# Optimization experiments

Measured on AMD Instinct MI355X. Metric: run time of the kernel, lower is better.

The kernel has to match this reference:

```python
import jax, jax.numpy as jnp
import numpy as np

B, S, H, NH, L = 2, 2048, 2048, 16, 512
HD = H // NH  # head_dim = 128


def setup_inputs() -> dict:
    key = jax.random.key(0)
    k1, k2, k3, k4, k5 = jax.random.split(key, 5)
    scale = 0.02  # mimic xavier-scale init
    return {
        "q": jax.random.normal(k1, (B, S, H), dtype=jnp.float32),
        "latent_kv": jax.random.normal(k2, (B, S, L), dtype=jnp.float32),
        "Wq": jax.random.normal(k3, (H, H), dtype=jnp.float32) * scale,
        "Wkv_expand": jax.random.normal(k4, (2 * H, L), dtype=jnp.float32) * scale,
        "Wout": jax.random.normal(k5, (H, H), dtype=jnp.float32) * scale,
    }


def reference(q, latent_kv, Wq, Wkv_expand, Wout):
    b, sq, _ = q.shape
    sk = latent_kv.shape[1]
    # projections (torch Linear: x @ W.T)
    qp = q @ Wq.T                              # [B,Sq,H]
    kv = latent_kv @ Wkv_expand.T              # [B,Sk,2H]
    k, v = jnp.split(kv, 2, axis=-1)           # each [B,Sk,H]
    # split heads -> [B,NH,S,HD]
    qh = qp.reshape(b, sq, NH, HD).transpose(0, 2, 1, 3)
    kh = k.reshape(b, sk, NH, HD).transpose(0, 2, 1, 3)
    vh = v.reshape(b, sk, NH, HD).transpose(0, 2, 1, 3)
    inv_sqrt_d = 1.0 / jnp.sqrt(jnp.float32(HD))
    scores = jnp.einsum("bhqd,bhkd->bhqk", qh, kh) * inv_sqrt_d
    # causal mask (seq_q == seq_k)
    causal = jnp.tril(jnp.ones((sq, sk), dtype=bool))
    scores = jnp.where(causal, scores, jnp.finfo(scores.dtype).min)
    attn = jax.nn.softmax(scores, axis=-1)
    out = jnp.einsum("bhqk,bhkd->bhqd", attn, vh)  # [B,NH,Sq,HD]
    out = out.transpose(0, 2, 1, 3).reshape(b, sq, H)
    return out @ Wout.T
```

## Files before the change

### kernel.cpp

```cpp
#include <hip/hip_runtime.h>

#define SLEN 2048
#define NHEADS 16
#define HDIM 128

typedef __attribute__((ext_vector_type(8))) short bf16x8;
typedef __attribute__((ext_vector_type(4))) float f32x4;
typedef __attribute__((ext_vector_type(16))) float f32x16;

__device__ __forceinline__ unsigned short f2bf(float f) {
  union { float f; unsigned u; } v; v.f = f;
  unsigned r = v.u + 0x7FFFu + ((v.u >> 16) & 1u);
  return (unsigned short)(r >> 16);
}

__device__ __forceinline__ float bf2f(unsigned short h) {
  union { unsigned u; float f; } v; v.u = (unsigned)h << 16;
  return v.f;
}

__device__ __forceinline__ unsigned pkbf(float a, float b) {
  unsigned r;
  asm("v_cvt_pk_bf16_f32 %0, %1, %2" : "=v"(r) : "v"(a), "v"(b));
  return r;
}

__device__ __forceinline__ void gload16(const void* g, void* l) {
  __builtin_amdgcn_global_load_lds(
      (const __attribute__((address_space(1))) unsigned int*)g,
      (__attribute__((address_space(3))) unsigned int*)l, 16, 0, 0);
}

__global__ __launch_bounds__(256) void cvt_all(const float* __restrict__ q,
                                               const float* __restrict__ Wq,
                                               const float* __restrict__ lat,
                                               const float* __restrict__ Wkv,
                                               const float* __restrict__ Wout,
                                               unsigned short* __restrict__ qo,
                                               unsigned short* __restrict__ Wqo,
                                               unsigned short* __restrict__ lato,
                                               unsigned short* __restrict__ Wkvo,
                                               unsigned short* __restrict__ Wouto) {
  const int blk = blockIdx.x;
  const float* in;
  unsigned short* out;
  int base;
  if (blk < 4096)      { in = q;    out = qo;    base = 0; }
  else if (blk < 6144) { in = Wq;   out = Wqo;   base = 4096; }
  else if (blk < 7168) { in = lat;  out = lato;  base = 6144; }
  else if (blk < 8192) { in = Wkv;  out = Wkvo;  base = 7168; }
  else                 { in = Wout; out = Wouto; base = 8192; }
  const int i = (blk - base) * 256 + threadIdx.x;
  const float4* p = reinterpret_cast<const float4*>(in) + (size_t)i * 2;
  float4 a = p[0], b = p[1];
  uint4 o;
  o.x = (unsigned)f2bf(a.x) | ((unsigned)f2bf(a.y) << 16);
  o.y = (unsigned)f2bf(a.z) | ((unsigned)f2bf(a.w) << 16);
  o.z = (unsigned)f2bf(b.x) | ((unsigned)f2bf(b.y) << 16);
  o.w = (unsigned)f2bf(b.z) | ((unsigned)f2bf(b.w) << 16);
  reinterpret_cast<uint4*>(out)[i] = o;
}

template <bool OUT_F32>
__global__ __launch_bounds__(256) void gemm_bt(const unsigned short* __restrict__ A,
                                               const unsigned short* __restrict__ B,
                                               void* __restrict__ Cv,
                                               int M, int N, int K,
                                               size_t zB, size_t zC, float scale) {
  __shared__ unsigned short As[128 * 32];
  __shared__ unsigned short Bs[128 * 32];
  const int tid = threadIdx.x;
  const int lane = tid & 63, wid = tid >> 6;
  const int g = lane >> 4, q = lane & 15;
  const int nbx = N >> 7;
  const int bx = blockIdx.x % nbx, by = blockIdx.x / nbx;
  const int tM = by << 7, tN = bx << 7;
  const int wm = (wid >> 1) * 64, wn = (wid & 1) * 64;
  const size_t zoff = (size_t)blockIdx.z;
  B += zoff * zB;

  f32x4 acc[4][4] = {};

  const int o0 = tid * 16;
  const int r0 = o0 >> 6, c0 = (o0 & 63) >> 1;
  const int r1 = r0 + 64;
  const unsigned short* gA0 = A + (size_t)(tM + r0) * K + c0;
  const unsigned short* gA1 = A + (size_t)(tM + r1) * K + c0;
  const unsigned short* gB0 = B + (size_t)(tN + r0) * K + c0;
  const unsigned short* gB1 = B + (size_t)(tN + r1) * K + c0;
  char* lA = (char*)As;
  char* lB = (char*)Bs;
  const int wo = wid * 1024;

  for (int kt = 0; kt < K; kt += 32) {
    gload16(gA0, lA + wo);
    gload16(gA1, lA + 4096 + wo);
    gload16(gB0, lB + wo);
    gload16(gB1, lB + 4096 + wo);
    gA0 += 32; gA1 += 32; gB0 += 32; gB1 += 32;
    __syncthreads();
    bf16x8 af[4], bfr[4];
#pragma unroll
    for (int i = 0; i < 4; ++i)
      af[i] = *(const bf16x8*)&As[(wm + i * 16 + q) * 32 + g * 8];
#pragma unroll
    for (int j = 0; j < 4; ++j)
      bfr[j] = *(const bf16x8*)&Bs[(wn + j * 16 + q) * 32 + g * 8];
#pragma unroll
    for (int i = 0; i < 4; ++i)
#pragma unroll
      for (int j = 0; j < 4; ++j)
        acc[i][j] = __builtin_amdgcn_mfma_f32_16x16x32_bf16(af[i], bfr[j], acc[i][j], 0, 0, 0);
    __syncthreads();
  }

  if constexpr (OUT_F32) {
    float* C = (float*)Cv + zoff * zC;
#pragma unroll
    for (int i = 0; i < 4; ++i)
#pragma unroll
      for (int j = 0; j < 4; ++j)
#pragma unroll
        for (int r = 0; r < 4; ++r)
          C[(size_t)(tM + wm + i * 16 + g * 4 + r) * N + (tN + wn + j * 16 + q)] =
              acc[i][j][r] * scale;
  } else {
    unsigned short* C = (unsigned short*)Cv + zoff * zC;
#pragma unroll
    for (int i = 0; i < 4; ++i)
#pragma unroll
      for (int j = 0; j < 4; ++j)
#pragma unroll
        for (int r = 0; r < 4; ++r)
          C[(size_t)(tM + wm + i * 16 + g * 4 + r) * N + (tN + wn + j * 16 + q)] =
              f2bf(acc[i][j][r] * scale);
  }
}

__global__ __launch_bounds__(256, 2) void mla_attn(const unsigned short* __restrict__ Q,
                                                   const unsigned short* __restrict__ K,
                                                   const unsigned short* __restrict__ VT,
                                                   unsigned short* __restrict__ Opart,
                                                   float* __restrict__ Stats) {
  __shared__ unsigned short Ks[2][64 * 128];
  __shared__ unsigned short Vs[2][128 * 64];

  const int tid = threadIdx.x, lane = tid & 63, w = tid >> 6;
  const int q5 = lane & 31, half = lane >> 5, q7 = lane & 7;
  const int s = blockIdx.x & 1;
  const int pr = (blockIdx.x >> 1) & 7;
  const int bh = blockIdx.x >> 4;
  const int head = bh & 15, b = bh >> 4;

  const unsigned short* Kbase = K + (size_t)(b * 2048) * 2048 + head * 128;
  const unsigned short* Vbase = VT + (size_t)(b * 2048 + head * 128) * 2048;

  const int r0 = tid >> 4, c0 = tid & 15;
  const unsigned short* kS = Kbase + (size_t)r0 * 2048 + ((c0 ^ r0) << 3);
  const int d0 = tid >> 3, c3 = tid & 7;
  const unsigned short* vS = Vbase + (size_t)d0 * 2048 + ((c3 ^ (d0 & 7)) << 3);

  const int arow0 = q5 * 256;
  const int vrow0 = q5 * 128;
  const int q15 = q5 & 15;

  for (int t2 = 0; t2 < 2; ++t2) {
    const int qt = t2 ? pr : 15 - pr;
    const int kt0 = s * (qt + 1);
    const int ktN = kt0 + qt + 1;
    const int myq = qt * 128 + w * 32 + q5;
    const unsigned short* Qrow = Q + (size_t)(b * 2048 + myq) * 2048 + head * 128;

    bf16x8 qf[8];
#pragma unroll
    for (int ks = 0; ks < 8; ++ks)
      qf[ks] = *(const bf16x8*)((const char*)Qrow + ks * 32 + half * 16);

    __syncthreads();

    {
      const int kvb0 = kt0 * 64;
      unsigned short* kd = &Ks[kt0 & 1][0] + tid * 8;
      unsigned short* vd = &Vs[kt0 & 1][0] + tid * 8;
      const unsigned short* ks2 = kS + (size_t)kvb0 * 2048;
      const unsigned short* vs2 = vS + kvb0;
#pragma unroll
      for (int u = 0; u < 4; ++u) gload16(ks2 + (size_t)u * 16 * 2048, kd + u * 2048);
#pragma unroll
      for (int u = 0; u < 4; ++u) gload16(vs2 + (size_t)u * 32 * 2048, vd + u * 2048);
    }

    float m2 = -1e30f, l = 0.f;
    f32x16 o[4];
#pragma unroll
    for (int i = 0; i < 16; ++i) { o[0][i] = 0.f; o[1][i] = 0.f; o[2][i] = 0.f; o[3][i] = 0.f; }

    for (int kt = kt0; kt < ktN; ++kt) {
      const int cur = kt & 1;
      asm volatile("s_waitcnt vmcnt(4)" ::: "memory");
      __builtin_amdgcn_s_barrier();

      if (kt + 1 < ktN) {
        const int kvb2 = (kt + 1) * 64;
        unsigned short* kd = &Ks[cur ^ 1][0] + tid * 8;
        unsigned short* vd = &Vs[cur ^ 1][0] + tid * 8;
        const unsigned short* ks2 = kS + (size_t)kvb2 * 2048;
        const unsigned short* vs2 = vS + kvb2;
#pragma unroll
        for (int u = 0; u < 4; ++u) gload16(ks2 + (size_t)u * 16 * 2048, kd + u * 2048);
#pragma unroll
        for (int u = 0; u < 4; ++u) gload16(vs2 + (size_t)u * 32 * 2048, vd + u * 2048);
      }

      f32x16 st[2];
#pragma unroll
      for (int i = 0; i < 16; ++i) { st[0][i] = 0.f; st[1][i] = 0.f; }
      const char* kb = (const char*)&Ks[cur][0];
      __builtin_amdgcn_s_setprio(1);
#pragma unroll
      for (int ks = 0; ks < 8; ++ks) {
        const int cd = ks * 2 + half;
#pragma unroll
        for (int m = 0; m < 2; ++m) {
          bf16x8 kf = *(const bf16x8*)(kb + arow0 + m * 8192 + ((cd ^ q15) << 4));
          st[m] = __builtin_amdgcn_mfma_f32_32x32x16_bf16(kf, qf[ks], st[m], 0, 0, 0);
        }
      }
      __builtin_amdgcn_s_setprio(0);

      float t[32];
      const int kvb = kt * 64;
      const bool needmask = (kvb + 63 > qt * 128 + w * 32);
#pragma unroll
      for (int m = 0; m < 2; ++m)
#pragma unroll
        for (int r = 0; r < 16; ++r) {
          float sv = st[m][r];
          if (needmask) {
            const int kvloc = m * 32 + (r & 3) + 8 * (r >> 2) + 4 * half;
            sv = (kvb + kvloc <= myq) ? sv : -3e38f;
          }
          t[m * 16 + r] = sv;
        }
      float mx = fmaxf(t[0], t[1]);
#pragma unroll
      for (int i = 2; i < 32; i += 2) mx = fmaxf(fmaxf(mx, t[i]), t[i + 1]);
      mx = fmaxf(mx, __shfl_xor(mx, 32));

      if (!__all(mx <= m2 + 11.54f)) {
        const float mnew = fmaxf(m2, mx);
        const float rsc = __builtin_amdgcn_exp2f(m2 - mnew);
        m2 = mnew; l *= rsc;
#pragma unroll
        for (int r = 0; r < 16; ++r) {
          const int rowv = (r & 3) + 8 * (r >> 2) + 4 * half;
          const float f = __shfl(rsc, rowv);
          o[0][r] *= f; o[1][r] *= f; o[2][r] *= f; o[3][r] *= f;
        }
      }

      float ts = 0.f;
#pragma unroll
      for (int i = 0; i < 32; ++i) { t[i] = __builtin_amdgcn_exp2f(t[i] - m2); ts += t[i]; }
      ts += __shfl_xor(ts, 32);
      l += ts;

      unsigned wpk[2][4][2];
#pragma unroll
      for (int m = 0; m < 2; ++m)
#pragma unroll
        for (int r4 = 0; r4 < 4; ++r4) {
          wpk[m][r4][0] = pkbf(t[m * 16 + r4 * 4 + 0], t[m * 16 + r4 * 4 + 1]);
          wpk[m][r4][1] = pkbf(t[m * 16 + r4 * 4 + 2], t[m * 16 + r4 * 4 + 3]);
        }

      if (kt + 1 < ktN) asm volatile("s_waitcnt vmcnt(8)" ::: "memory");
      else              asm volatile("s_waitcnt vmcnt(0)" ::: "memory");
      __builtin_amdgcn_s_barrier();

      const char* vb = (const char*)&Vs[cur][0];
#pragma unroll
      for (int ks = 0; ks < 4; ++ks) {
        const int m = ks >> 1, i = ks & 1;
        const unsigned s0 = half ? wpk[m][2 * i][0] : wpk[m][2 * i + 1][0];
        const unsigned s1 = half ? wpk[m][2 * i][1] : wpk[m][2 * i + 1][1];
        const unsigned rv0 = (unsigned)__shfl_xor((int)s0, 32);
        const unsigned rv1 = (unsigned)__shfl_xor((int)s1, 32);
        const unsigned ow0 = half ? wpk[m][2 * i + 1][0] : wpk[m][2 * i][0];
        const unsigned ow1 = half ? wpk[m][2 * i + 1][1] : wpk[m][2 * i][1];
        union { unsigned u[4]; bf16x8 v; } fr;
        fr.u[0] = half ? rv0 : ow0;
        fr.u[1] = half ? rv1 : ow1;
        fr.u[2] = half ? ow0 : rv0;
        fr.u[3] = half ? ow1 : rv1;
        const int cd = ks * 2 + half;
        __builtin_amdgcn_s_setprio(1);
#pragma unroll
        for (int nf = 0; nf < 4; ++nf) {
          bf16x8 vf = *(const bf16x8*)(vb + vrow0 + nf * 4096 + ((cd ^ q7) << 4));
          o[nf] = __builtin_amdgcn_mfma_f32_32x32x16_bf16(fr.v, vf, o[nf], 0, 0, 0);
        }
        __builtin_amdgcn_s_setprio(0);
      }
    }

    const int set = (bh * 16 + qt) * 2 + s;
    const int base_o = set << 14;
    const int base_s = set << 8;
    if (half == 0) {
      Stats[base_s + (w * 32 + q5) * 2] = m2;
      Stats[base_s + (w * 32 + q5) * 2 + 1] = l;
    }
#pragma unroll
    for (int r = 0; r < 16; ++r) {
      const int rowv = (r & 3) + 8 * (r >> 2) + 4 * half;
      const int row = w * 32 + rowv;
#pragma unroll
      for (int nf = 0; nf < 4; ++nf)
        Opart[base_o + row * 128 + nf * 32 + q5] = f2bf(o[nf][r]);
    }
  }
}

__global__ __launch_bounds__(256) void mla_merge(const unsigned short* __restrict__ Op,
                                                 const float* __restrict__ St,
                                                 unsigned short* __restrict__ AO) {
  const int idx = blockIdx.x * 256 + threadIdx.x;
  const int rid = idx >> 4;
  const int d0 = (idx & 15) << 3;
  const int bhqt = rid >> 7;
  const int row = rid & 127;
  const int sb = bhqt << 1;
  const float m1 = St[(sb << 8) + row * 2];
  const float l1 = St[(sb << 8) + row * 2 + 1];
  const float m2 = St[(sb << 8) + 256 + row * 2];
  const float l2 = St[(sb << 8) + 256 + row * 2 + 1];
  const float M = fmaxf(m1, m2);
  const float w1 = __builtin_amdgcn_exp2f(m1 - M);
  const float w2 = __builtin_amdgcn_exp2f(m2 - M);
  const float inv = 1.0f / (w1 * l1 + w2 * l2);
  const unsigned short* p1 = Op + ((size_t)sb << 14) + row * 128 + d0;
  bf16x8 a = *(const bf16x8*)p1;
  bf16x8 c = *(const bf16x8*)(p1 + 16384);
  const int bh = bhqt >> 4, qt = bhqt & 15;
  const int head = bh & 15, b = bh >> 4;
  unsigned short outv[8];
#pragma unroll
  for (int j = 0; j < 8; ++j)
    outv[j] = f2bf((w1 * bf2f((unsigned short)a[j]) + w2 * bf2f((unsigned short)c[j])) * inv);
  unsigned short* dst = AO + ((size_t)(b * 2048 + qt * 128 + row)) * 2048 + head * 128 + d0;
  *(uint4*)dst = *(const uint4*)outv;
}

extern "C" void kernel_launch(void* const* d_in, const int* in_sizes, int n_in,
                              void* d_out, int out_size, void* d_ws, size_t ws_size,
                              hipStream_t stream) {
  const float* q    = (const float*)d_in[0];
  const float* lat  = (const float*)d_in[1];
  const float* Wq   = (const float*)d_in[2];
  const float* Wkv  = (const float*)d_in[3];
  const float* Wout = (const float*)d_in[4];

  char* ws = (char*)d_ws;
  unsigned short* qbf   = (unsigned short*)(ws);
  unsigned short* Opart = (unsigned short*)(ws);
  unsigned short* Wqbf  = (unsigned short*)(ws + 16777216);
  unsigned short* latbf = (unsigned short*)(ws + 25165824);
  unsigned short* Wkvbf = (unsigned short*)(ws + 29360128);
  unsigned short* Wobf  = (unsigned short*)(ws + 33554432);
  unsigned short* qpbf  = (unsigned short*)(ws + 41943040);
  unsigned short* Kbf   = (unsigned short*)(ws + 58720256);
  unsigned short* aobf  = (unsigned short*)(ws + 58720256);
  unsigned short* VTbf  = (unsigned short*)(ws + 75497472);
  float*          Stats = (float*)(ws + 92274688);
  unsigned short* Wvbf  = Wkvbf + (size_t)2048 * 512;

  const float SCALE_L2E = 0.12751742f;

  cvt_all<<<10240, 256, 0, stream>>>(q, Wq, lat, Wkv, Wout,
                                     qbf, Wqbf, latbf, Wkvbf, Wobf);

  gemm_bt<false><<<512, 256, 0, stream>>>(qbf, Wqbf, qpbf, 4096, 2048, 2048, 0, 0, SCALE_L2E);
  gemm_bt<false><<<512, 256, 0, stream>>>(latbf, Wkvbf, Kbf, 4096, 2048, 512, 0, 0, 1.0f);
  gemm_bt<false><<<dim3(256, 1, 2), 256, 0, stream>>>(
      Wvbf, latbf, VTbf, 2048, 2048, 512,
      (size_t)2048 * 512, (size_t)2048 * 2048, 1.0f);
  mla_attn<<<512, 256, 0, stream>>>(qpbf, Kbf, VTbf, Opart, Stats);
  mla_merge<<<4096, 256, 0, stream>>>(Opart, Stats, aobf);
  gemm_bt<true><<<512, 256, 0, stream>>>(aobf, Wobf, (float*)d_out, 4096, 2048, 2048, 0, 0, 1.0f);
}
```

Baseline: 234.3 us.

## Pipeline GEMM global-to-LDS loads with 4-stage ring buffer and XOR swizzle

```diff
diff --git a/kernel.cpp b/kernel.cpp
--- a/kernel.cpp
+++ b/kernel.cpp
@@ -62,56 +62,71 @@
 }
 
 template <bool OUT_F32>
-__global__ __launch_bounds__(256) void gemm_bt(const unsigned short* __restrict__ A,
-                                               const unsigned short* __restrict__ B,
-                                               void* __restrict__ Cv,
-                                               int M, int N, int K,
-                                               size_t zB, size_t zC, float scale) {
-  __shared__ unsigned short As[128 * 32];
-  __shared__ unsigned short Bs[128 * 32];
+__global__ __launch_bounds__(256, 2) void gemm_bt(const unsigned short* __restrict__ A,
+                                                  const unsigned short* __restrict__ B,
+                                                  void* __restrict__ Cv,
+                                                  int M, int N, int K,
+                                                  size_t zB, size_t zC, float scale) {
+  __shared__ unsigned short As[4][128 * 32];
+  __shared__ unsigned short Bs[4][128 * 32];
   const int tid = threadIdx.x;
   const int lane = tid & 63, wid = tid >> 6;
   const int g = lane >> 4, q = lane & 15;
   const int nbx = N >> 7;
-  const int bx = blockIdx.x % nbx, by = blockIdx.x / nbx;
+  const int cpx = gridDim.x >> 3;
+  const int bid = (blockIdx.x & 7) * cpx + (blockIdx.x >> 3);
+  const int bx = bid % nbx, by = bid / nbx;
   const int tM = by << 7, tN = bx << 7;
   const int wm = (wid >> 1) * 64, wn = (wid & 1) * 64;
   const size_t zoff = (size_t)blockIdx.z;
   B += zoff * zB;
 
+  const int sr = tid >> 2, sc = tid & 3;
+  const int scs = sc ^ (sr & 3);
+  const unsigned short* gA0 = A + (size_t)(tM + sr) * K + (scs << 3);
+  const unsigned short* gA1 = A + (size_t)(tM + 64 + sr) * K + (scs << 3);
+  const unsigned short* gB0 = B + (size_t)(tN + sr) * K + (scs << 3);
+  const unsigned short* gB1 = B + (size_t)(tN + 64 + sr) * K + (scs << 3);
+
+  const int nk = K >> 5;
+  const int gq = g ^ (q & 3);
+
+  auto STAGE = [&](int slot, int kt) {
+    const size_t ko = (size_t)kt << 5;
+    unsigned short* ad = &As[slot][0] + tid * 8;
+    unsigned short* bd = &Bs[slot][0] + tid * 8;
+    gload16(gA0 + ko, ad);
+    gload16(gA1 + ko, ad + 2048);
+    gload16(gB0 + ko, bd);
+    gload16(gB1 + ko, bd + 2048);
+  };
+
+  STAGE(0, 0); STAGE(1, 1); STAGE(2, 2);
+
   f32x4 acc[4][4] = {};
 
-  const int o0 = tid * 16;
-  const int r0 = o0 >> 6, c0 = (o0 & 63) >> 1;
-  const int r1 = r0 + 64;
-  const unsigned short* gA0 = A + (size_t)(tM + r0) * K + c0;
-  const unsigned short* gA1 = A + (size_t)(tM + r1) * K + c0;
-  const unsigned short* gB0 = B + (size_t)(tN + r0) * K + c0;
-  const unsigned short* gB1 = B + (size_t)(tN + r1) * K + c0;
-  char* lA = (char*)As;
-  char* lB = (char*)Bs;
-  const int wo = wid * 1024;
-
-  for (int kt = 0; kt < K; kt += 32) {
-    gload16(gA0, lA + wo);
-    gload16(gA1, lA + 4096 + wo);
-    gload16(gB0, lB + wo);
-    gload16(gB1, lB + 4096 + wo);
-    gA0 += 32; gA1 += 32; gB0 += 32; gB1 += 32;
-    __syncthreads();
+  for (int t = 0; t < nk; ++t) {
+    if (t + 2 < nk)      asm volatile("s_waitcnt vmcnt(8)" ::: "memory");
+    else if (t + 1 < nk) asm volatile("s_waitcnt vmcnt(4)" ::: "memory");
+    else                 asm volatile("s_waitcnt vmcnt(0)" ::: "memory");
+    __builtin_amdgcn_s_barrier();
+    if (t + 3 < nk) STAGE((t + 3) & 3, t + 3);
+
+    const int s = t & 3;
     bf16x8 af[4], bfr[4];
 #pragma unroll
     for (int i = 0; i < 4; ++i)
-      af[i] = *(const bf16x8*)&As[(wm + i * 16 + q) * 32 + g * 8];
+      af[i] = *(const bf16x8*)&As[s][(wm + i * 16 + q) * 32 + gq * 8];
 #pragma unroll
     for (int j = 0; j < 4; ++j)
-      bfr[j] = *(const bf16x8*)&Bs[(wn + j * 16 + q) * 32 + g * 8];
+      bfr[j] = *(const bf16x8*)&Bs[s][(wn + j * 16 + q) * 32 + gq * 8];
+    __builtin_amdgcn_s_setprio(1);
 #pragma unroll
     for (int i = 0; i < 4; ++i)
 #pragma unroll
       for (int j = 0; j < 4; ++j)
         acc[i][j] = __builtin_amdgcn_mfma_f32_16x16x32_bf16(af[i], bfr[j], acc[i][j], 0, 0, 0);
-    __syncthreads();
+    __builtin_amdgcn_s_setprio(0);
   }
 
   if constexpr (OUT_F32) {
```

Result: faster. 222.3 us, median of 3 (-5.1%).
